# Kernel optimization log

Hardware: AMD Instinct MI355X
Metric: run time of the kernel (lower is better)

Reference implementation:

```python
import jax, jax.numpy as jnp
import numpy as np

N = 50000   # nodes
E = 800000  # edges
D = 128     # input_size == hidden_size
R = 4       # n_relations
L = 3       # n_layers


def setup_inputs() -> dict:
    key = jax.random.key(0)
    ks = jax.random.split(key, 8)
    x = jax.random.normal(ks[0], (N, D), dtype=jnp.float32)
    edge_index = jax.random.randint(ks[1], (2, E), 0, N, dtype=jnp.int32)
    edge_type = jax.random.randint(ks[2], (E,), 0, R, dtype=jnp.int32)
    scale = 1.0 / np.sqrt(D)
    W = jax.random.normal(ks[3], (L, R, D, D), dtype=jnp.float32) * scale      # per-relation weights
    root = jax.random.normal(ks[4], (L, D, D), dtype=jnp.float32) * scale      # root (self) weights
    bias = jnp.zeros((L, D), dtype=jnp.float32)
    gamma = jnp.ones((L, D), dtype=jnp.float32)   # LayerNorm weight
    beta = jnp.zeros((L, D), dtype=jnp.float32)   # LayerNorm bias
    return {"x": x, "edge_index": edge_index, "edge_type": edge_type,
            "W": W, "root": root, "bias": bias, "gamma": gamma, "beta": beta}


def _rgcn_conv(x, src, dst, etype, W_r, W_root, b):
    # Transform all nodes by every relation weight once: [R, N, D]
    h = jnp.einsum('ni,rio->rno', x, W_r)
    msg = h[etype, src]                                   # [E, D] per-edge messages
    # mean aggregation per (dst, relation), matching PyG RGCNConv aggr='mean'
    seg = dst * R + etype                                 # combined segment id
    cnt = jax.ops.segment_sum(jnp.ones((E,), x.dtype), seg, num_segments=N * R)
    inv = 1.0 / jnp.maximum(cnt, 1.0)
    agg = jax.ops.segment_sum(msg * inv[seg][:, None], dst, num_segments=N)
    return agg + x @ W_root + b


def _layernorm(x, g, b, eps=1e-5):
    mu = jnp.mean(x, axis=-1, keepdims=True)
    var = jnp.var(x, axis=-1, keepdims=True)
    return (x - mu) * jax.lax.rsqrt(var + eps) * g + b


def reference(x, edge_index, edge_type, W, root, bias, gamma, beta):
    src, dst = edge_index[0], edge_index[1]
    for i in range(L):
        x_res = x
        x = _rgcn_conv(x, src, dst, edge_type, W[i], root[i], bias[i])
        x = jax.nn.relu(x)
        # dropout p=0.0 -> no-op; residual_projection is Identity (input_size==hidden_size)
        x = x + x_res
        x = _layernorm(x, gamma[i], beta[i])
    return x
```

## Files before the change

kernel.cpp:

```cpp
#include <hip/hip_runtime.h>
#include <stdint.h>

#define NN 50000
#define EE 800000
#define DD 128
#define RR 4
#define LL 3
#define NRSEG (NN*RR)
#define NKB 20
#define NB_SCAN ((NRSEG + 1023)/1024)
#define NBK NB_SCAN
#define BKCAP 5120
#define WCONV_T (LL*NKB*8*64)

typedef _Float16 f16;
typedef _Float16 f16x8 __attribute__((ext_vector_type(8)));
typedef float f32x4 __attribute__((ext_vector_type(4)));

union U32H { uint32_t u; f16 h[2]; };
union U4H  { uint4 u; f16 h[8]; };

__global__ __launch_bounds__(1024) void k_binA(const int* __restrict__ ei, const int* __restrict__ et,
                                               int* __restrict__ cnt, int* __restrict__ bcur,
                                               uint2* __restrict__ tmp){
  __shared__ int bcnt[NBK];
  __shared__ int bbase[NBK];
  int t = threadIdx.x;
  if(t < NBK) bcnt[t] = 0;
  __syncthreads();

  int e = blockIdx.x*1024 + t;
  int seg = -1, src = 0, bk = 0, rk = 0;
  if(e < EE){
    src = ei[e];
    seg = ei[EE+e]*RR + et[e];
    bk  = seg >> 10;
    rk  = atomicAdd(&bcnt[bk], 1);
    atomicAdd(&cnt[seg], 1);
  }
  __syncthreads();
  if(t < NBK){
    int c = bcnt[t];
    bbase[t] = (c > 0) ? atomicAdd(&bcur[t], c) : 0;
  }
  __syncthreads();
  if(seg >= 0){
    uint2 p; p.x = (uint32_t)seg; p.y = (uint32_t)src;
    tmp[(size_t)bk*BKCAP + bbase[bk] + rk] = p;
  }
}

__global__ __launch_bounds__(256) void k_scan(const int* __restrict__ cnt, const int* __restrict__ bcur,
                                              int* __restrict__ rowp){
  __shared__ int s[256];
  int b = blockIdx.x, t = threadIdx.x;

  int v = (t < NBK) ? bcur[t] : 0;
  s[t] = (t < b) ? v : 0;
  __syncthreads();
  for(int o=128;o>0;o>>=1){ if(t<o) s[t]+=s[t+o]; __syncthreads(); }
  int boff_b = s[0];
  __syncthreads();

  if(b == NBK-1){
    s[t] = v;
    __syncthreads();
    for(int o=128;o>0;o>>=1){ if(t<o) s[t]+=s[t+o]; __syncthreads(); }
    if(t==0) rowp[NRSEG] = s[0];
    __syncthreads();
  }

  int base = b*1024 + t*4;
  int c[4]; int tot=0;
  #pragma unroll
  for(int j=0;j<4;j++){ int i=base+j; c[j] = (i<NRSEG)? cnt[i]:0; tot+=c[j]; }
  s[t]=tot; __syncthreads();
  for(int o=1;o<256;o<<=1){ int x=(t>=o)?s[t-o]:0; __syncthreads(); s[t]+=x; __syncthreads(); }
  int run = boff_b + s[t]-tot;
  #pragma unroll
  for(int j=0;j<4;j++){
    int i=base+j;
    if(i<NRSEG){ rowp[i]=run; run+=c[j]; }
  }
}

__global__ __launch_bounds__(1024) void k_binB(const int* __restrict__ rowp, const int* __restrict__ bcur,
                                               const uint2* __restrict__ tmp, int* __restrict__ ssrc){
  __shared__ int lcur[1024];
  int b = blockIdx.x, t = threadIdx.x;
  lcur[t] = 0;
  __syncthreads();
  int n = bcur[b];
  const uint2* src = tmp + (size_t)b*BKCAP;
  for(int i = t; i < n; i += 1024){
    uint2 p = src[i];
    int pos = rowp[p.x] + atomicAdd(&lcur[p.x & 1023], 1);
    ssrc[pos] = (int)p.y;
  }
}

__global__ __launch_bounds__(256) void k_convWX(const float* __restrict__ W, const float* __restrict__ root,
                                                f16* __restrict__ Wf,
                                                const float* __restrict__ x, f16* __restrict__ x16){
  int t = blockIdx.x*256 + threadIdx.x;
  if(t < WCONV_T){
    int lane = t & 63;
    int cb   = (t>>6) & 7;
    int kb   = (t>>9) % NKB;
    int l    = (t>>9) / NKB;
    int col  = cb*16 + (lane&15);
    int kbase= kb*32 + (lane>>4)*8;
    f16* dst = Wf + (size_t)t*8;
    #pragma unroll
    for(int e=0;e<8;e++){
      int k = kbase+e;
      float v = (k < 4*DD) ? W[(((size_t)l*RR + (k>>7))*DD + (k&127))*DD + col]
                           : root[((size_t)l*DD + (k-4*DD))*DD + col];
      dst[e] = (f16)v;
    }
  } else {
    int u = t - WCONV_T;
    if(u < NN*DD/8){
      const float4* xf = (const float4*)x + (size_t)u*2;
      float4 a = xf[0], b = xf[1];
      U4H o;
      o.h[0]=(f16)a.x; o.h[1]=(f16)a.y; o.h[2]=(f16)a.z; o.h[3]=(f16)a.w;
      o.h[4]=(f16)b.x; o.h[5]=(f16)b.y; o.h[6]=(f16)b.z; o.h[7]=(f16)b.w;
      ((uint4*)x16)[u] = o.u;
    }
  }
}

__device__ __forceinline__ void acc8(float a[8], uint4 v){
  U4H w; w.u = v;
  #pragma unroll
  for(int k=0;k<8;k++) a[k] += (float)w.h[k];
}

__global__ __launch_bounds__(256) void k_agg(const f16* __restrict__ x16, const int* __restrict__ rowp,
                                             const int* __restrict__ ssrc, f16* __restrict__ A16){
  int seg = blockIdx.x*16 + (threadIdx.x >> 4);
  int l   = threadIdx.x & 15;
  if(seg >= NRSEG) return;

  int b = rowp[seg], e = rowp[seg+1];
  int n = e - b;
  const uint4* xl = (const uint4*)x16 + l;

  float acc[8];
  #pragma unroll
  for(int k=0;k<8;k++) acc[k] = 0.f;

  for(int base=0; base<n; base+=4){
    int m = n - base;
    int i0 = b + base;
    int c0 = ssrc[i0];
    int c1 = (m>1) ? ssrc[i0+1] : c0;
    int c2 = (m>2) ? ssrc[i0+2] : c0;
    int c3 = (m>3) ? ssrc[i0+3] : c0;
    uint4 v0 = xl[(size_t)c0*16];
    uint4 v1 = xl[(size_t)c1*16];
    uint4 v2 = xl[(size_t)c2*16];
    uint4 v3 = xl[(size_t)c3*16];
    acc8(acc, v0);
    if(m>1) acc8(acc, v1);
    if(m>2) acc8(acc, v2);
    if(m>3) acc8(acc, v3);
  }

  float inv = 1.f/(float)max(n,1);
  U4H o;
  #pragma unroll
  for(int k=0;k<8;k++) o.h[k] = (f16)(acc[k]*inv);
  ((uint4*)A16)[(size_t)seg*16 + l] = o.u;
}

__device__ __forceinline__ void stageB(const f16* __restrict__ Wf, f16* lds, int kb, int wid, int lane){
  const f16* src = Wf + (size_t)kb*4096;
  #pragma unroll
  for(int j=wid;j<8;j+=4){
    __builtin_amdgcn_global_load_lds((const __attribute__((address_space(1))) void*)(src + j*512 + lane*8),
                                     (__attribute__((address_space(3))) void*)(lds + j*512), 16, 0, 0);
  }
}

template<int LAST>
__global__ __launch_bounds__(256) void k_gemm(const f16* __restrict__ A16, const f16* __restrict__ x16,
                                              const f16* __restrict__ Wf,
                                              const float* __restrict__ bias, const float* __restrict__ gmm,
                                              const float* __restrict__ bet,
                                              f16* __restrict__ xnext, float* __restrict__ outf){
  __shared__ f16 Blds[2][4096];
  int tid  = threadIdx.x;
  int lane = tid & 63, wid = tid >> 6;
  int rbase = blockIdx.x*128 + wid*32;
  int fr = lane & 15, kg = lane >> 4;

  int arow0 = rbase + fr;       if(arow0 >= NN) arow0 = NN-1;
  int arow1 = rbase + 16 + fr;  if(arow1 >= NN) arow1 = NN-1;
  const f16* Ar0 = A16 + (size_t)arow0*512 + kg*8;
  const f16* Ar1 = A16 + (size_t)arow1*512 + kg*8;
  const f16* Xr0 = x16 + (size_t)arow0*128 + kg*8;
  const f16* Xr1 = x16 + (size_t)arow1*128 + kg*8;

  f32x4 acc[2][8];
  #pragma unroll
  for(int r=0;r<2;r++)
    #pragma unroll
    for(int c=0;c<8;c++) acc[r][c] = (f32x4){0.f,0.f,0.f,0.f};

  f16x8 a0, a1;
  a0 = *(const f16x8*)(Ar0); a1 = *(const f16x8*)(Ar1);
  stageB(Wf, &Blds[0][0], 0, wid, lane);

  for(int kb=0; kb<NKB; kb++){
    __syncthreads();
    if(kb+1 < NKB) stageB(Wf, &Blds[(kb+1)&1][0], kb+1, wid, lane);
    f16x8 na0 = a0, na1 = a1;
    if(kb+1 < NKB){
      if(kb+1 < 16){ na0 = *(const f16x8*)(Ar0 + (kb+1)*32); na1 = *(const f16x8*)(Ar1 + (kb+1)*32); }
      else         { na0 = *(const f16x8*)(Xr0 + (kb+1-16)*32); na1 = *(const f16x8*)(Xr1 + (kb+1-16)*32); }
    }
    const f16* bb = &Blds[kb&1][lane*8];
    #pragma unroll
    for(int cb=0;cb<8;cb++){
      f16x8 b = *(const f16x8*)(bb + cb*512);
      acc[0][cb] = __builtin_amdgcn_mfma_f32_16x16x32_f16(a0, b, acc[0][cb], 0, 0, 0);
      acc[1][cb] = __builtin_amdgcn_mfma_f32_16x16x32_f16(a1, b, acc[1][cb], 0, 0, 0);
    }
    a0 = na0; a1 = na1;
  }

  float bs[8];
  #pragma unroll
  for(int cb=0;cb<8;cb++) bs[cb] = bias[cb*16 + fr];
  int g4 = kg*4;
  #pragma unroll
  for(int rh=0; rh<2; rh++){
    float vv[8][4];
    #pragma unroll
    for(int cb=0;cb<8;cb++){
      int col = cb*16 + fr;
      #pragma unroll
      for(int q=0;q<4;q++){
        float v = acc[rh][cb][q] + bs[cb];
        v = v > 0.f ? v : 0.f;
        int row = rbase + rh*16 + g4 + q;
        float res = (row < NN) ? (float)x16[(size_t)row*128 + col] : 0.f;
        vv[cb][q] = v + res;
      }
    }
    #pragma unroll
    for(int q=0;q<4;q++){
      float s1=0.f, s2=0.f;
      #pragma unroll
      for(int cb=0;cb<8;cb++){ float v=vv[cb][q]; s1+=v; s2+=v*v; }
      #pragma unroll
      for(int m=1;m<16;m<<=1){ s1 += __shfl_xor(s1,m,16); s2 += __shfl_xor(s2,m,16); }
      float mu  = s1*(1.f/128.f);
      float var = s2*(1.f/128.f) - mu*mu;
      float rs  = rsqrtf(var + 1e-5f);
      int row = rbase + rh*16 + g4 + q;
      if(row < NN){
        #pragma unroll
        for(int cb=0;cb<8;cb++){
          int col = cb*16 + fr;
          float y = (vv[cb][q]-mu)*rs*gmm[col] + bet[col];
          if(LAST) outf[(size_t)row*128 + col] = y;
          else     xnext[(size_t)row*128 + col] = (f16)y;
        }
      }
    }
  }
}

extern "C" void kernel_launch(void* const* d_in, const int* in_sizes, int n_in,
                              void* d_out, int out_size, void* d_ws, size_t ws_size,
                              hipStream_t stream){
  const float* x    = (const float*)d_in[0];
  const int*   ei   = (const int*)d_in[1];
  const int*   et   = (const int*)d_in[2];
  const float* W    = (const float*)d_in[3];
  const float* root = (const float*)d_in[4];
  const float* bias = (const float*)d_in[5];
  const float* gmm  = (const float*)d_in[6];
  const float* bet  = (const float*)d_in[7];

  char* ws = (char*)d_ws;
  int*   cnt  = (int*)(ws + 0);
  int*   bcur = (int*)(ws + 800000);
  int*   rowp = (int*)(ws + 801792);
  int*   ssrc = (int*)(ws + 1604096);
  f16*   Wf   = (f16*)(ws + 4804608);
  f16*   x16a = (f16*)(ws + 5296128);
  f16*   x16b = (f16*)(ws + 18096128);
  f16*   A16  = (f16*)(ws + 30896128);
  uint2* tmp  = (uint2*)A16;

  hipMemsetAsync(cnt, 0, 800784, stream);
  k_binA  <<<(EE+1023)/1024, 1024, 0, stream>>>(ei, et, cnt, bcur, tmp);
  k_scan  <<<NB_SCAN, 256, 0, stream>>>(cnt, bcur, rowp);
  k_binB  <<<NBK, 1024, 0, stream>>>(rowp, bcur, tmp, ssrc);
  k_convWX<<<(WCONV_T + NN*DD/8 + 255)/256, 256, 0, stream>>>(W, root, Wf, x, x16a);

  f16* xc = x16a; f16* xn = x16b;
  for(int l=0; l<LL; l++){
    k_agg<<<NRSEG/16, 256, 0, stream>>>(xc, rowp, ssrc, A16);
    if(l < LL-1)
      k_gemm<0><<<(NN+127)/128, 256, 0, stream>>>(A16, xc, Wf + (size_t)l*81920,
                                                  bias+l*DD, gmm+l*DD, bet+l*DD, xn, nullptr);
    else
      k_gemm<1><<<(NN+127)/128, 256, 0, stream>>>(A16, xc, Wf + (size_t)l*81920,
                                                  bias+l*DD, gmm+l*DD, bet+l*DD, nullptr, (float*)d_out);
    f16* t = xc; xc = xn; xn = t;
  }
}
```

Before: 266.6 us.

## Restructure CSR build: local-staged binning, per-bucket histogram scan, drop global counts

The edge binning that builds the CSR is reorganized. k_binA now handles 4096 edges per block, scans its bucket counts and stages entries in shared memory so the global writes to bucket storage are grouped. The global per-segment count array and its memset are removed: k_binB builds a per-bucket histogram in LDS, scans it to produce rowp directly, then scatters the sources. A tiny single-block prefix kernel replaces the multi-block k_scan. This cuts global atomics and the 800KB memset, at the cost of a second pass over each bucket in k_binB and a heavier k_binA.

Result: faster. 228.0 us (-14.4%).

```diff
diff --git a/kernel.cpp b/kernel.cpp
--- a/kernel.cpp
+++ b/kernel.cpp
@@ -8,8 +8,7 @@
 #define LL 3
 #define NRSEG (NN*RR)
 #define NKB 20
-#define NB_SCAN ((NRSEG + 1023)/1024)
-#define NBK NB_SCAN
+#define NBK 196
 #define BKCAP 5120
 #define WCONV_T (LL*NKB*8*64)
 
@@ -21,81 +20,101 @@
 union U4H  { uint4 u; f16 h[8]; };
 
 __global__ __launch_bounds__(1024) void k_binA(const int* __restrict__ ei, const int* __restrict__ et,
-                                               int* __restrict__ cnt, int* __restrict__ bcur,
-                                               uint2* __restrict__ tmp){
-  __shared__ int bcnt[NBK];
-  __shared__ int bbase[NBK];
+                                               int* __restrict__ bcur, int2* __restrict__ tmp){
+  __shared__ int bcnt[256];
+  __shared__ int lbase[256];
+  __shared__ int gbase[256];
+  __shared__ int s[256];
+  __shared__ int tot;
+  __shared__ int2 stage[4096];
   int t = threadIdx.x;
-  if(t < NBK) bcnt[t] = 0;
-  __syncthreads();
-
-  int e = blockIdx.x*1024 + t;
-  int seg = -1, src = 0, bk = 0, rk = 0;
-  if(e < EE){
-    src = ei[e];
-    seg = ei[EE+e]*RR + et[e];
-    bk  = seg >> 10;
-    rk  = atomicAdd(&bcnt[bk], 1);
-    atomicAdd(&cnt[seg], 1);
-  }
-  __syncthreads();
-  if(t < NBK){
-    int c = bcnt[t];
-    bbase[t] = (c > 0) ? atomicAdd(&bcur[t], c) : 0;
-  }
-  __syncthreads();
-  if(seg >= 0){
-    uint2 p; p.x = (uint32_t)seg; p.y = (uint32_t)src;
-    tmp[(size_t)bk*BKCAP + bbase[bk] + rk] = p;
-  }
-}
-
-__global__ __launch_bounds__(256) void k_scan(const int* __restrict__ cnt, const int* __restrict__ bcur,
-                                              int* __restrict__ rowp){
+  if(t < 256) bcnt[t] = 0;
+  __syncthreads();
+
+  int seg[4], src[4], bk[4], rk[4];
+  #pragma unroll
+  for(int j=0;j<4;j++){
+    int e = blockIdx.x*4096 + j*1024 + t;
+    if(e < EE){
+      src[j] = ei[e];
+      seg[j] = ei[EE+e]*RR + et[e];
+      bk[j]  = seg[j] >> 10;
+      rk[j]  = atomicAdd(&bcnt[bk[j]], 1);
+    } else { seg[j] = -1; }
+  }
+  __syncthreads();
+
+  if(t < 256) s[t] = bcnt[t];
+  __syncthreads();
+  for(int o=1;o<256;o<<=1){
+    int x = (t<256 && t>=o) ? s[t-o] : 0;
+    __syncthreads();
+    if(t<256) s[t] += x;
+    __syncthreads();
+  }
+  if(t < 256){
+    lbase[t] = s[t] - bcnt[t];
+    if(t == 255) tot = s[255];
+    if(t < NBK && bcnt[t] > 0) gbase[t] = atomicAdd(&bcur[t], bcnt[t]);
+  }
+  __syncthreads();
+
+  #pragma unroll
+  for(int j=0;j<4;j++){
+    if(seg[j] >= 0){
+      int2 p; p.x = seg[j]; p.y = src[j];
+      stage[lbase[bk[j]] + rk[j]] = p;
+    }
+  }
+  __syncthreads();
+
+  int T = tot;
+  #pragma unroll
+  for(int j=0;j<4;j++){
+    int idx = j*1024 + t;
+    if(idx < T){
+      int2 p = stage[idx];
+      int bb = p.x >> 10;
+      tmp[(size_t)bb*BKCAP + gbase[bb] + (idx - lbase[bb])] = p;
+    }
+  }
+}
+
+__global__ __launch_bounds__(256) void k_prefix(const int* __restrict__ bcur, int* __restrict__ boff){
   __shared__ int s[256];
+  int t = threadIdx.x;
+  int v = (t < NBK) ? bcur[t] : 0;
+  s[t] = v; __syncthreads();
+  for(int o=1;o<256;o<<=1){ int x=(t>=o)?s[t-o]:0; __syncthreads(); s[t]+=x; __syncthreads(); }
+  if(t < NBK) boff[t] = s[t] - v;
+}
+
+__global__ __launch_bounds__(1024) void k_binB(const int* __restrict__ boff, const int* __restrict__ bcur,
+                                               const int2* __restrict__ tmp,
+                                               int* __restrict__ rowp, int* __restrict__ ssrc){
+  __shared__ int hist[1024];
+  __shared__ int sc[1024];
+  __shared__ int cur[1024];
   int b = blockIdx.x, t = threadIdx.x;
-
-  int v = (t < NBK) ? bcur[t] : 0;
-  s[t] = (t < b) ? v : 0;
-  __syncthreads();
-  for(int o=128;o>0;o>>=1){ if(t<o) s[t]+=s[t+o]; __syncthreads(); }
-  int boff_b = s[0];
-  __syncthreads();
-
-  if(b == NBK-1){
-    s[t] = v;
-    __syncthreads();
-    for(int o=128;o>0;o>>=1){ if(t<o) s[t]+=s[t+o]; __syncthreads(); }
-    if(t==0) rowp[NRSEG] = s[0];
-    __syncthreads();
-  }
-
-  int base = b*1024 + t*4;
-  int c[4]; int tot=0;
-  #pragma unroll
-  for(int j=0;j<4;j++){ int i=base+j; c[j] = (i<NRSEG)? cnt[i]:0; tot+=c[j]; }
-  s[t]=tot; __syncthreads();
-  for(int o=1;o<256;o<<=1){ int x=(t>=o)?s[t-o]:0; __syncthreads(); s[t]+=x; __syncthreads(); }
-  int run = boff_b + s[t]-tot;
-  #pragma unroll
-  for(int j=0;j<4;j++){
-    int i=base+j;
-    if(i<NRSEG){ rowp[i]=run; run+=c[j]; }
-  }
-}
-
-__global__ __launch_bounds__(1024) void k_binB(const int* __restrict__ rowp, const int* __restrict__ bcur,
-                                               const uint2* __restrict__ tmp, int* __restrict__ ssrc){
-  __shared__ int lcur[1024];
-  int b = blockIdx.x, t = threadIdx.x;
-  lcur[t] = 0;
+  hist[t] = 0;
   __syncthreads();
   int n = bcur[b];
-  const uint2* src = tmp + (size_t)b*BKCAP;
+  const int2* src = tmp + (size_t)b*BKCAP;
+  for(int i = t; i < n; i += 1024) atomicAdd(&hist[src[i].x & 1023], 1);
+  __syncthreads();
+  sc[t] = hist[t]; __syncthreads();
+  for(int o=1;o<1024;o<<=1){ int x=(t>=o)?sc[t-o]:0; __syncthreads(); sc[t]+=x; __syncthreads(); }
+  int gb = boff[b];
+  int excl = gb + sc[t] - hist[t];
+  cur[t] = excl;
+  int idx = b*1024 + t;
+  if(idx < NRSEG) rowp[idx] = excl;
+  if(b == NBK-1 && t == 0) rowp[NRSEG] = gb + sc[1023];
+  __syncthreads();
   for(int i = t; i < n; i += 1024){
-    uint2 p = src[i];
-    int pos = rowp[p.x] + atomicAdd(&lcur[p.x & 1023], 1);
-    ssrc[pos] = (int)p.y;
+    int2 p = src[i];
+    int pos = atomicAdd(&cur[p.x & 1023], 1);
+    ssrc[pos] = p.y;
   }
 }
 
@@ -287,20 +306,20 @@
   const float* bet  = (const float*)d_in[7];
 
   char* ws = (char*)d_ws;
-  int*   cnt  = (int*)(ws + 0);
-  int*   bcur = (int*)(ws + 800000);
-  int*   rowp = (int*)(ws + 801792);
-  int*   ssrc = (int*)(ws + 1604096);
-  f16*   Wf   = (f16*)(ws + 4804608);
-  f16*   x16a = (f16*)(ws + 5296128);
-  f16*   x16b = (f16*)(ws + 18096128);
-  f16*   A16  = (f16*)(ws + 30896128);
-  uint2* tmp  = (uint2*)A16;
-
-  hipMemsetAsync(cnt, 0, 800784, stream);
-  k_binA  <<<(EE+1023)/1024, 1024, 0, stream>>>(ei, et, cnt, bcur, tmp);
-  k_scan  <<<NB_SCAN, 256, 0, stream>>>(cnt, bcur, rowp);
-  k_binB  <<<NBK, 1024, 0, stream>>>(rowp, bcur, tmp, ssrc);
+  int*   bcur = (int*)(ws + 0);
+  int*   boff = (int*)(ws + 1024);
+  int*   rowp = (int*)(ws + 2048);
+  int*   ssrc = (int*)(ws + 804096);
+  f16*   Wf   = (f16*)(ws + 4004096);
+  f16*   x16a = (f16*)(ws + 4495616);
+  f16*   x16b = (f16*)(ws + 17295616);
+  f16*   A16  = (f16*)(ws + 30095616);
+  int2*  tmp  = (int2*)A16;
+
+  hipMemsetAsync(bcur, 0, 784, stream);
+  k_binA  <<<NBK, 1024, 0, stream>>>(ei, et, bcur, tmp);
+  k_prefix<<<1, 256, 0, stream>>>(bcur, boff);
+  k_binB  <<<NBK, 1024, 0, stream>>>(boff, bcur, tmp, rowp, ssrc);
   k_convWX<<<(WCONV_T + NN*DD/8 + 255)/256, 256, 0, stream>>>(W, root, Wf, x, x16a);
 
   f16* xc = x16a; f16* xn = x16b;
```
